# Kernel tuning notes

Measured on AMD Instinct MI355X. Metric: run time of the kernel, lower is better.

Reference implementation:

```python
import jax, jax.numpy as jnp
import numpy as np

B, N, D, H = 2, 2048, 1024, 16
HD = D // H  # 64
EPS = 1e-6


def setup_inputs() -> dict:
    key = jax.random.key(0)
    ks = jax.random.split(key, 16)
    rnd = lambda k, shp: jax.random.normal(k, shp, dtype=jnp.float32)
    w = lambda k, i, o: rnd(k, (i, o)) * 0.02  # stored as (in, out); y = x @ W
    return {
        "x": rnd(ks[0], (B, N, D)),
        "emb_B_D": rnd(ks[1], (B, D)),
        "gate": rnd(ks[2], (B, D)),
        "crossattn_emb": rnd(ks[3], (B, 128, D)),
        "rope_emb_L_1_1_D": rnd(ks[4], (N, HD)),
        "Wq1": w(ks[5], D, D), "Wq2": w(ks[6], D, D),
        "Wk1": w(ks[7], D, D), "Wk2": w(ks[8], D, D),
        "Wv": w(ks[9], D, D),
        "Wo": w(ks[10], D, D),
        "Wada1": w(ks[11], D, D),
        "Wada2": w(ks[12], D, 2 * D),
        "bada2": jnp.zeros((2 * D,), dtype=jnp.float32),
    }


def rotate_half(t):
    t1, t2 = jnp.split(t, 2, axis=-1)
    return jnp.concatenate([-t2, t1], axis=-1)


def reference(x, emb_B_D, gate, crossattn_emb, rope_emb_L_1_1_D,
              Wq1, Wq2, Wk1, Wk2, Wv, Wo, Wada1, Wada2, bada2):
    # adaLN modulation: SiLU -> Linear(no bias) -> Linear(bias)
    ada = jax.nn.silu(emb_B_D) @ Wada1 @ Wada2 + bada2          # [B, 2D]
    shift, scale = jnp.split(ada, 2, axis=1)                    # [B, D] each

    # LayerNorm (no affine) + scale/shift
    mu = jnp.mean(x, axis=-1, keepdims=True)
    var = jnp.var(x, axis=-1, keepdims=True)
    xn = (x - mu) * jax.lax.rsqrt(var + EPS)
    xn = xn * (1.0 + scale[:, None, :]) + shift[:, None, :]     # [B, N, D]

    # QKV projections (each to_q/to_k is two stacked linears, to_v one)
    q = xn @ Wq1 @ Wq2
    k = xn @ Wk1 @ Wk2
    v = xn @ Wv
    split_heads = lambda t: t.reshape(B, N, H, HD).transpose(0, 2, 1, 3)  # b h n d
    q, k, v = split_heads(q), split_heads(k), split_heads(v)

    # RoPE
    cos = jnp.cos(rope_emb_L_1_1_D)[None, None]                 # [1,1,N,HD]
    sin = jnp.sin(rope_emb_L_1_1_D)[None, None]
    q = q * cos + rotate_half(q) * sin
    k = k * cos + rotate_half(k) * sin

    # Attention
    sim = jnp.einsum("bhid,bhjd->bhij", q, k) * (HD ** -0.5)
    attn = jax.nn.softmax(sim, axis=-1)
    out = jnp.einsum("bhij,bhjd->bhid", attn, v)
    out = out.transpose(0, 2, 1, 3).reshape(B, N, D) @ Wo

    # Gated residual
    return x + gate[:, None, :] * out
```

## Files before the change

kernel.cpp:

```cpp
#include <hip/hip_runtime.h>
#include <stdint.h>
#include <math.h>

typedef unsigned short u16;
typedef __attribute__((ext_vector_type(8))) short short8;
typedef __attribute__((ext_vector_type(4))) float f32x4;
typedef __attribute__((ext_vector_type(4))) unsigned short u16x4;
typedef __attribute__((ext_vector_type(2))) unsigned int uint2v;

#define DEV static __device__ __forceinline__

DEV u16 f2bf(float f) {
    unsigned u = __builtin_bit_cast(unsigned, f);
    u = u + 0x7fffu + ((u >> 16) & 1u);
    return (u16)(u >> 16);
}
DEV float bf2f(u16 s) { return __builtin_bit_cast(float, ((unsigned)s) << 16); }
DEV float fexp2(float x) {
#if __has_builtin(__builtin_amdgcn_exp2f)
    return __builtin_amdgcn_exp2f(x);
#else
    return __expf(x * 0.69314718056f);
#endif
}
DEV unsigned cvtpk(float a, float b) {
    unsigned w;
    asm("v_cvt_pk_bf16_f32 %0, %1, %2" : "=v"(w) : "v"(a), "v"(b));
    return w;
}
DEV int xcd_swz(int flat, int nwg) {
    int cpx = nwg >> 3;
    return (flat & 7) * cpx + (flat >> 3);
}

DEV void gl_lds16(const u16* g, u16* l) {
#if __has_builtin(__builtin_amdgcn_global_load_lds)
    __builtin_amdgcn_global_load_lds((const __attribute__((address_space(1))) unsigned int*)g,
                                     (__attribute__((address_space(3))) unsigned int*)l, 16, 0, 0);
#else
    *(short8*)l = *(const short8*)g;
#endif
}


__global__ __launch_bounds__(256) void k_ada1(const float* __restrict__ emb, const float* __restrict__ W,
                                              float* __restrict__ out) {
    int col = blockIdx.x * 64 + (threadIdx.x & 63);
    int b = blockIdx.y;
    int kbase = blockIdx.z * 128 + (threadIdx.x >> 6) * 32;
    float acc = 0.f;
    for (int k = kbase; k < kbase + 32; k++) {
        float e = emb[b * 1024 + k];
        float se = e / (1.f + __expf(-e));
        acc += se * W[(size_t)k * 1024 + col];
    }
    __shared__ float red[4][64];
    red[threadIdx.x >> 6][threadIdx.x & 63] = acc;
    __syncthreads();
    if (threadIdx.x < 64)
        atomicAdd(out + b * 1024 + blockIdx.x * 64 + threadIdx.x,
                  red[0][threadIdx.x] + red[1][threadIdx.x] + red[2][threadIdx.x] + red[3][threadIdx.x]);
}

__global__ __launch_bounds__(256) void k_prep(const float* s0, u16* d0, const float* s1, u16* d1,
                                              const float* s2, u16* d2, const float* s3, u16* d3,
                                              const float* s4, u16* d4, const float* s5, u16* d5,
                                              const float* __restrict__ t_ada, const float* __restrict__ Wada2,
                                              float* __restrict__ ada, const float* __restrict__ rope,
                                              float* __restrict__ cst, float* __restrict__ snt) {
    __shared__ u16 tile[64][65];
    __shared__ float red[4][64];
    if (blockIdx.z == 6) {
        int flat = blockIdx.y * 16 + blockIdx.x;
        int kq = flat >> 6;
        int rest = flat & 63;
        int b = rest >> 5, xb = rest & 31;
        int col = xb * 64 + (threadIdx.x & 63);
        int kbase = kq * 256 + (threadIdx.x >> 6) * 64;
        float acc = 0.f;
        for (int k = kbase; k < kbase + 64; k++)
            acc += t_ada[b * 1024 + k] * Wada2[(size_t)k * 2048 + col];
        red[threadIdx.x >> 6][threadIdx.x & 63] = acc;
        __syncthreads();
        if (threadIdx.x < 64)
            atomicAdd(ada + b * 2048 + xb * 64 + threadIdx.x,
                      red[0][threadIdx.x] + red[1][threadIdx.x] + red[2][threadIdx.x] + red[3][threadIdx.x]);
        return;
    }
    if (blockIdx.z == 7) {
        int flat = blockIdx.y * 16 + blockIdx.x;
        if (flat < 128) {
            int idx = flat * 1024 + threadIdx.x * 4;
            float4 rv = *(const float4*)(rope + idx);
            float4 cv, sv;
            __sincosf(rv.x, &sv.x, &cv.x);
            __sincosf(rv.y, &sv.y, &cv.y);
            __sincosf(rv.z, &sv.z, &cv.z);
            __sincosf(rv.w, &sv.w, &cv.w);
            *(float4*)(cst + idx) = cv;
            *(float4*)(snt + idx) = sv;
        }
        return;
    }
    const float* s; u16* d;
    switch (blockIdx.z) {
        case 0: s = s0; d = d0; break;
        case 1: s = s1; d = d1; break;
        case 2: s = s2; d = d2; break;
        case 3: s = s3; d = d3; break;
        case 4: s = s4; d = d4; break;
        default: s = s5; d = d5; break;
    }
    int k0 = blockIdx.x * 64, n0 = blockIdx.y * 64;
    int tx = threadIdx.x & 63, ty = threadIdx.x >> 6;
    if (blockIdx.z >= 4) {
        #pragma unroll
        for (int i = 0; i < 16; i++) {
            int kk = ty + 4 * i;
            d[(size_t)(k0 + kk) * 1024 + n0 + tx] = f2bf(s[(size_t)(k0 + kk) * 1024 + n0 + tx]);
        }
        return;
    }
    #pragma unroll
    for (int i = 0; i < 16; i++) {
        int kk = ty + 4 * i;
        tile[kk][tx] = f2bf(s[(size_t)(k0 + kk) * 1024 + n0 + tx]);
    }
    __syncthreads();
    #pragma unroll
    for (int i = 0; i < 16; i++) {
        int nn = ty + 4 * i;
        d[(size_t)(n0 + nn) * 1024 + k0 + tx] = tile[tx][nn];
    }
}

__global__ __launch_bounds__(256) void k_ln(const float* __restrict__ x, const float* __restrict__ ada,
                                            const float* __restrict__ bada2, u16* __restrict__ xn) {
    int row = blockIdx.x;
    int b = row >> 11;
    float4 v = ((const float4*)(x + (size_t)row * 1024))[threadIdx.x];
    float s = v.x + v.y + v.z + v.w;
    float ss = v.x * v.x + v.y * v.y + v.z * v.z + v.w * v.w;
    #pragma unroll
    for (int m = 1; m < 64; m <<= 1) { s += __shfl_xor(s, m, 64); ss += __shfl_xor(ss, m, 64); }
    __shared__ float red[2][4];
    int wave = threadIdx.x >> 6, lane = threadIdx.x & 63;
    if (lane == 0) { red[0][wave] = s; red[1][wave] = ss; }
    __syncthreads();
    s = red[0][0] + red[0][1] + red[0][2] + red[0][3];
    ss = red[1][0] + red[1][1] + red[1][2] + red[1][3];
    float mu = s * (1.f / 1024.f);
    float var = ss * (1.f / 1024.f) - mu * mu;
    float rs = rsqrtf(var + 1e-6f);
    int c = threadIdx.x * 4;
    const float* sh = ada + b * 2048;
    const float* sc = ada + b * 2048 + 1024;
    u16x4 r;
    r.x = f2bf((v.x - mu) * rs * (1.f + sc[c + 0] + bada2[1024 + c + 0]) + sh[c + 0] + bada2[c + 0]);
    r.y = f2bf((v.y - mu) * rs * (1.f + sc[c + 1] + bada2[1024 + c + 1]) + sh[c + 1] + bada2[c + 1]);
    r.z = f2bf((v.z - mu) * rs * (1.f + sc[c + 2] + bada2[1024 + c + 2]) + sh[c + 2] + bada2[c + 2]);
    r.w = f2bf((v.w - mu) * rs * (1.f + sc[c + 3] + bada2[1024 + c + 3]) + sh[c + 3] + bada2[c + 3]);
    *(u16x4*)(xn + (size_t)row * 1024 + c) = r;
}

template <int BM, int BN, int MODE>
DEV void gemm_core(const u16* __restrict__ A, const u16* __restrict__ Bt,
                   u16* __restrict__ Cb, float* __restrict__ Cf, u16* __restrict__ Vt,
                   const float* __restrict__ Xres, const float* __restrict__ gate,
                   const float* __restrict__ cst, const float* __restrict__ snt,
                   float scale, int Nn, int K, int m0, int n0) {
    constexpr int MI = BM / 32, NJ = BN / 32;
    constexpr int PA = BM / 64, PB = BN / 64;
    constexpr int LA = BM * 32, LB = BN * 32;
    constexpr int SST = 2 * (LA + LB);
    constexpr int SM = (MODE == 2 && BM * 132 > SST) ? BM * 132 : SST;
    __shared__ u16 smem[SM];
    int tid = threadIdx.x;
    int lane = tid & 63, wave = tid >> 6;
    int wm = (wave & 1) * (BM / 2), wn = (wave >> 1) * (BN / 2);
    int lr = lane & 15, quad = lane >> 4;
    f32x4 acc[MI][NJ];
    #pragma unroll
    for (int i = 0; i < MI; i++)
        #pragma unroll
        for (int j = 0; j < NJ; j++) acc[i][j] = f32x4{0.f, 0.f, 0.f, 0.f};

    int arow = tid >> 2;
    int achunk = (tid & 3) * 8;
    const u16* ap = A + (size_t)(m0 + arow) * K + achunk;
    const u16* bp = Bt + (size_t)(n0 + arow) * K + achunk;

    auto stage = [&](int it, int d) {
        int koff = it * 32;
        int ab = d * LA, bb = 2 * LA + d * LB;
        #pragma unroll
        for (int p = 0; p < PA; p++)
            gl_lds16(ap + koff + (size_t)(64 * p) * K, smem + ab + (arow + 64 * p) * 32 + achunk);
        #pragma unroll
        for (int p = 0; p < PB; p++)
            gl_lds16(bp + koff + (size_t)(64 * p) * K, smem + bb + (arow + 64 * p) * 32 + achunk);
    };

    stage(0, 0);
    __syncthreads();
    #pragma unroll 1
    for (int it = 0; it < 32; ++it) {
        int cur = it & 1;
        if (it + 1 < 32) stage(it + 1, cur ^ 1);
        int ab = cur * LA, bb = 2 * LA + cur * LB;
        short8 af[MI], bfr[NJ];
        #pragma unroll
        for (int i = 0; i < MI; i++)
            af[i] = *(const short8*)(smem + ab + (wm + i * 16 + lr) * 32 + quad * 8);
        #pragma unroll
        for (int j = 0; j < NJ; j++)
            bfr[j] = *(const short8*)(smem + bb + (wn + j * 16 + lr) * 32 + quad * 8);
        #pragma unroll
        for (int i = 0; i < MI; i++)
            #pragma unroll
            for (int j = 0; j < NJ; j++)
                acc[i][j] = __builtin_amdgcn_mfma_f32_16x16x32_bf16(af[i], bfr[j], acc[i][j], 0, 0, 0);
        __syncthreads();
    }

    if (MODE == 2) {
        if ((n0 + wn) < 2048) {
            #pragma unroll
            for (int i = 0; i < MI; i++)
                #pragma unroll
                for (int jp = 0; jp < 2; jp++)
                    #pragma unroll
                    for (int r = 0; r < 4; r++) {
                        int row = m0 + wm + i * 16 + quad * 4 + r;
                        int n = row & 2047;
                        int d1 = jp * 16 + lr;
                        float c1 = cst[n * 64 + d1],      s1 = snt[n * 64 + d1];
                        float c2 = cst[n * 64 + d1 + 32], s2 = snt[n * 64 + d1 + 32];
                        float x1 = acc[i][jp][r], x2 = acc[i][jp + 2][r];
                        Cb[(size_t)row * Nn + n0 + wn + d1]      = f2bf(x1 * c1 - x2 * s1);
                        Cb[(size_t)row * Nn + n0 + wn + d1 + 32] = f2bf(x2 * c2 + x1 * s2);
                    }
        } else {
            #pragma unroll
            for (int i = 0; i < MI; i++)
                #pragma unroll
                for (int j = 0; j < NJ; j++) {
                    u16x4 w;
                    w.x = f2bf(acc[i][j][0]); w.y = f2bf(acc[i][j][1]);
                    w.z = f2bf(acc[i][j][2]); w.w = f2bf(acc[i][j][3]);
                    *(u16x4*)(&smem[(wn + j * 16 + lr) * 132 + wm + i * 16 + quad * 4]) = w;
                }
            __syncthreads();
            int d = tid >> 1, half = tid & 1;
            int gcol = n0 - 2048 + d;
            int hv = gcol >> 6, dl = gcol & 63;
            int bb2 = m0 >> 11;
            int nloc = (m0 & 2047) + half * 64;
            u16* dst = Vt + ((size_t)((bb2 * 16 + hv) * 64 + dl)) * 2048 + nloc;
            #pragma unroll
            for (int c = 0; c < 8; c++)
                *(short8*)(dst + c * 8) = *(const short8*)(&smem[d * 132 + half * 64 + c * 8]);
        }
        return;
    }
    #pragma unroll
    for (int i = 0; i < MI; i++)
        #pragma unroll
        for (int j = 0; j < NJ; j++)
            #pragma unroll
            for (int r = 0; r < 4; r++) {
                int row = m0 + wm + i * 16 + quad * 4 + r;
                int col = n0 + wn + j * 16 + lr;
                float v = acc[i][j][r];
                if (MODE == 1) {
                    int b = row >> 11;
                    Cf[(size_t)row * Nn + col] = Xres[(size_t)row * Nn + col] + gate[b * 1024 + col] * v;
                } else {
                    Cb[(size_t)row * Nn + col] = f2bf(v * scale);
                }
            }
}

template <int BM, int BN, int MODE, int WPE>
__global__ __launch_bounds__(256, WPE) void gemm_bt(const u16* __restrict__ A, const u16* __restrict__ Bt,
                                                    u16* __restrict__ Cb, float* __restrict__ Cf,
                                                    u16* __restrict__ Vt,
                                                    const float* __restrict__ Xres, const float* __restrict__ gate,
                                                    const float* __restrict__ cst, const float* __restrict__ snt,
                                                    int Nn, int K) {
    int gx = gridDim.x;
    int flat = blockIdx.y * gx + blockIdx.x;
    int swz = xcd_swz(flat, gx * gridDim.y);
    gemm_core<BM, BN, MODE>(A, Bt, Cb, Cf, Vt, Xres, gate, cst, snt, 1.f, Nn, K,
                            (swz / gx) * BM, (swz % gx) * BN);
}

__global__ __launch_bounds__(256, 4) void gemm_fold(const u16* A0, const u16* B0, u16* C0,
                                                    const u16* A1, const u16* B1, u16* C1) {
    const u16* A = blockIdx.z ? A1 : A0;
    const u16* Bt = blockIdx.z ? B1 : B0;
    u16* C = blockIdx.z ? C1 : C0;
    float scale = blockIdx.z ? 1.0f : 0.18033688f;
    int flat = blockIdx.y * 16 + blockIdx.x;
    int swz = xcd_swz(flat, 128);
    gemm_core<128, 64, 0>(A, Bt, C, nullptr, nullptr, nullptr, nullptr, nullptr, nullptr, scale,
                          1024, 1024, (swz >> 4) * 128, (swz & 15) * 64);
}

__global__ __launch_bounds__(512) void k_attn(const u16* __restrict__ qkv, const u16* __restrict__ vt,
                                              u16* __restrict__ aob) {
    __shared__ u16 pool[128 * 72];
    __shared__ u16 Ks[2][64][64];
    __shared__ u16 Vs[2][64][64];
    int flat = blockIdx.y * 16 + blockIdx.x;
    int swz = xcd_swz(flat, 512);
    int q0 = (swz & 15) * 128;
    int bh = swz >> 4; int b = bh >> 4, h = bh & 15;
    int tid = threadIdx.x;
    int lane = tid & 63, wave = tid >> 6;
    int lr = lane & 15, quad = lane >> 4;
    int srow = tid >> 3, scol = (tid & 7) * 8;
    int sg = (((tid & 7) ^ (srow & 7))) * 8;
    int cc[2] = { ((quad ^ (lr & 7))) * 8, (((4 + quad) ^ (lr & 7))) * 8 };
    int qrow = wave * 16 + lr;

    const u16* kp = qkv + ((size_t)(b * 2048 + srow)) * 2048 + 1024 + h * 64 + sg;
    const u16* vp = vt + ((size_t)(bh * 64 + srow)) * 2048 + sg;

    #pragma unroll
    for (int p = 0; p < 2; p++)
        gl_lds16(qkv + ((size_t)(b * 2048 + q0 + srow + 64 * p)) * 2048 + h * 64 + sg,
                 pool + (srow + 64 * p) * 64 + scol);

    short8 krA, vrA, krB, vrB;
    krA = *(const short8*)(kp);
    vrA = *(const short8*)(vp);
    __syncthreads();
    short8 qf[2];
    #pragma unroll
    for (int ks = 0; ks < 2; ks++)
        qf[ks] = *(const short8*)(pool + qrow * 64 + cc[ks]);
    *(short8*)(&Ks[0][srow][scol]) = krA;
    *(short8*)(&Vs[0][srow][scol]) = vrA;
    krB = *(const short8*)(kp + (size_t)64 * 2048);
    vrB = *(const short8*)(vp + 64);
    __syncthreads();

    float l_part = 0.f;
    f32x4 oacc[4];
    #pragma unroll
    for (int dt = 0; dt < 4; dt++) oacc[dt] = f32x4{0.f, 0.f, 0.f, 0.f};

    auto body = [&](int it, int cur, short8& krF, short8& vrF, short8& krH, short8& vrH) {
        if (it < 30) {
            krF = *(const short8*)(kp + (size_t)(it + 2) * 64 * 2048);
            vrF = *(const short8*)(vp + (it + 2) * 64);
        }
        f32x4 st[4];
        #pragma unroll
        for (int ct = 0; ct < 4; ct++) st[ct] = f32x4{0.f, 0.f, 0.f, 0.f};
        #pragma unroll
        for (int ks = 0; ks < 2; ks++) {
            short8 kf[4];
            #pragma unroll
            for (int ct = 0; ct < 4; ct++)
                kf[ct] = *(const short8*)(&Ks[cur][ct * 16 + lr][cc[ks]]);
            __builtin_amdgcn_s_setprio(1);
            #pragma unroll
            for (int ct = 0; ct < 4; ct++)
                st[ct] = __builtin_amdgcn_mfma_f32_16x16x32_bf16(kf[ct], qf[ks], st[ct], 0, 0, 0);
            __builtin_amdgcn_s_setprio(0);
        }
        #pragma unroll
        for (int ct = 0; ct < 4; ct++) {
            float p0 = fexp2(st[ct][0]);
            float p1 = fexp2(st[ct][1]);
            float p2 = fexp2(st[ct][2]);
            float p3 = fexp2(st[ct][3]);
            l_part += (p0 + p1) + (p2 + p3);
            uint2v w; w.x = cvtpk(p0, p1); w.y = cvtpk(p2, p3);
            *(uint2v*)(pool + qrow * 72 + ct * 16 + quad * 4) = w;
        }
        #pragma unroll
        for (int ks = 0; ks < 2; ks++) {
            short8 pf, vf[4];
            pf = *(const short8*)(pool + qrow * 72 + ks * 32 + quad * 8);
            #pragma unroll
            for (int dt = 0; dt < 4; dt++)
                vf[dt] = *(const short8*)(&Vs[cur][dt * 16 + lr][cc[ks]]);
            __builtin_amdgcn_s_setprio(1);
            #pragma unroll
            for (int dt = 0; dt < 4; dt++)
                oacc[dt] = __builtin_amdgcn_mfma_f32_16x16x32_bf16(pf, vf[dt], oacc[dt], 0, 0, 0);
            __builtin_amdgcn_s_setprio(0);
        }
        if (it < 31) {
            int nxt = cur ^ 1;
            *(short8*)(&Ks[nxt][srow][scol]) = krH;
            *(short8*)(&Vs[nxt][srow][scol]) = vrH;
        }
        __syncthreads();
    };

    #pragma unroll 1
    for (int it2 = 0; it2 < 16; ++it2) {
        body(2 * it2,     0, krA, vrA, krB, vrB);
        body(2 * it2 + 1, 1, krB, vrB, krA, vrA);
    }

    float l = l_part;
    l += __shfl_xor(l, 16, 64);
    l += __shfl_xor(l, 32, 64);
    float linv[4];
    #pragma unroll
    for (int r = 0; r < 4; r++)
        linv[r] = 1.f / __shfl(l, quad * 4 + r, 64);
    #pragma unroll
    for (int dt = 0; dt < 4; dt++)
        #pragma unroll
        for (int r = 0; r < 4; r++) {
            int row = q0 + wave * 16 + quad * 4 + r;
            aob[((size_t)(b * 2048 + row)) * 1024 + h * 64 + dt * 16 + lr] =
                f2bf(oacc[dt][r] * linv[r]);
        }
}

extern "C" void kernel_launch(void* const* d_in, const int* in_sizes, int n_in,
                              void* d_out, int out_size, void* d_ws, size_t ws_size,
                              hipStream_t stream) {
    const float* x     = (const float*)d_in[0];
    const float* emb   = (const float*)d_in[1];
    const float* gate  = (const float*)d_in[2];
    const float* rope  = (const float*)d_in[4];
    const float* Wq1   = (const float*)d_in[5];
    const float* Wq2   = (const float*)d_in[6];
    const float* Wk1   = (const float*)d_in[7];
    const float* Wk2   = (const float*)d_in[8];
    const float* Wv    = (const float*)d_in[9];
    const float* Wo    = (const float*)d_in[10];
    const float* Wada1 = (const float*)d_in[11];
    const float* Wada2 = (const float*)d_in[12];
    const float* bada2 = (const float*)d_in[13];
    float* out = (float*)d_out;

    char* ws = (char*)d_ws;
    size_t off = 0;
    auto alloc = [&](size_t bytes) { void* p = ws + off; off += (bytes + 255) & ~(size_t)255; return p; };
    float* t_ada = (float*)alloc(2048 * 4);
    float* ada   = (float*)alloc(4096 * 4);
    float* cst   = (float*)alloc((size_t)131072 * 4);
    float* snt   = (float*)alloc((size_t)131072 * 4);
    u16* xn    = (u16*)alloc((size_t)4096 * 1024 * 2);
    u16* Wq1b  = (u16*)alloc((size_t)1024 * 1024 * 2);
    u16* Wk1b  = (u16*)alloc((size_t)1024 * 1024 * 2);
    u16* Wq2t  = (u16*)alloc((size_t)1024 * 1024 * 2);
    u16* Wk2t  = (u16*)alloc((size_t)1024 * 1024 * 2);
    u16* Wot   = (u16*)alloc((size_t)1024 * 1024 * 2);
    u16* WqkvT = (u16*)alloc((size_t)3072 * 1024 * 2);
    u16* qkvb  = (u16*)alloc((size_t)4096 * 2048 * 2);
    u16* vtb   = (u16*)alloc((size_t)4096 * 1024 * 2);
    u16* aob   = (u16*)alloc((size_t)4096 * 1024 * 2);
    (void)ws_size; (void)in_sizes; (void)n_in; (void)out_size;

    hipMemsetAsync(t_ada, 0, 2048 * 4, stream);
    hipMemsetAsync(ada, 0, 4096 * 4, stream);

    k_ada1<<<dim3(16, 2, 8), 256, 0, stream>>>(emb, Wada1, t_ada);

    k_prep<<<dim3(16, 16, 8), 256, 0, stream>>>(Wq2, Wq2t, Wk2, Wk2t,
                                                Wv, WqkvT + (size_t)2048 * 1024, Wo, Wot,
                                                Wq1, Wq1b, Wk1, Wk1b,
                                                t_ada, Wada2, ada, rope, cst, snt);

    k_ln<<<4096, 256, 0, stream>>>(x, ada, bada2, xn);

    gemm_fold<<<dim3(16, 8, 2), 256, 0, stream>>>(Wq2t, Wq1b, WqkvT,
                                                  Wk2t, Wk1b, WqkvT + (size_t)1024 * 1024);

    gemm_bt<128, 128, 2, 4><<<dim3(24, 32), 256, 0, stream>>>(xn, WqkvT, qkvb, nullptr, vtb,
                                                              nullptr, nullptr, cst, snt, 2048, 1024);

    k_attn<<<dim3(16, 32), 512, 0, stream>>>(qkvb, vtb, aob);

    gemm_bt<128, 64, 1, 4><<<dim3(16, 32), 256, 0, stream>>>(aob, Wot, nullptr, out, nullptr, x, gate,
                                                             nullptr, nullptr, 1024, 1024);
}
```

Baseline: 256.5 us.

## Triple-buffer GEMM LDS stages with vmcnt-based waits and lighter barriers

The GEMM main loop moves from a double-buffered to a triple-buffered LDS pipeline. It issues global-to-LDS loads two k-steps ahead and waits with a partial vmcnt count, so one stage's loads can still be in flight at each barrier. The attention loop's __syncthreads is replaced by an explicit lgkmcnt(0) wait plus s_barrier, which avoids draining outstanding vector-memory loads. The cost is 1.5x more shared memory per GEMM block, which may lower occupancy, and the hand-written waitcnt logic must stay correct.

Measured after the change: 257.2 us. About the same (+0.3%).

```diff
diff --git a/kernel.cpp b/kernel.cpp
--- a/kernel.cpp
+++ b/kernel.cpp
@@ -40,6 +40,12 @@
 #else
     *(short8*)l = *(const short8*)g;
 #endif
+}
+
+DEV void barrier_lgkm() {
+    asm volatile("s_waitcnt lgkmcnt(0)" ::: "memory");
+    __builtin_amdgcn_sched_barrier(0);
+    __builtin_amdgcn_s_barrier();
 }
 
 
@@ -172,7 +178,8 @@
     constexpr int MI = BM / 32, NJ = BN / 32;
     constexpr int PA = BM / 64, PB = BN / 64;
     constexpr int LA = BM * 32, LB = BN * 32;
-    constexpr int SST = 2 * (LA + LB);
+    constexpr int LBUF = LA + LB;
+    constexpr int SST = 3 * LBUF;
     constexpr int SM = (MODE == 2 && BM * 132 > SST) ? BM * 132 : SST;
     __shared__ u16 smem[SM];
     int tid = threadIdx.x;
@@ -192,7 +199,7 @@
 
     auto stage = [&](int it, int d) {
         int koff = it * 32;
-        int ab = d * LA, bb = 2 * LA + d * LB;
+        int ab = d * LBUF, bb = d * LBUF + LA;
         #pragma unroll
         for (int p = 0; p < PA; p++)
             gl_lds16(ap + koff + (size_t)(64 * p) * K, smem + ab + (arow + 64 * p) * 32 + achunk);
@@ -202,12 +209,15 @@
     };
 
     stage(0, 0);
-    __syncthreads();
+    stage(1, 1);
+    asm volatile("s_waitcnt vmcnt(%0)" :: "i"(PA + PB) : "memory");
+    __builtin_amdgcn_sched_barrier(0);
+    __builtin_amdgcn_s_barrier();
     #pragma unroll 1
     for (int it = 0; it < 32; ++it) {
-        int cur = it & 1;
-        if (it + 1 < 32) stage(it + 1, cur ^ 1);
-        int ab = cur * LA, bb = 2 * LA + cur * LB;
+        int cur = it % 3;
+        if (it + 2 < 32) stage(it + 2, (it + 2) % 3);
+        int ab = cur * LBUF, bb = ab + LA;
         short8 af[MI], bfr[NJ];
         #pragma unroll
         for (int i = 0; i < MI; i++)
@@ -220,8 +230,16 @@
             #pragma unroll
             for (int j = 0; j < NJ; j++)
                 acc[i][j] = __builtin_amdgcn_mfma_f32_16x16x32_bf16(af[i], bfr[j], acc[i][j], 0, 0, 0);
-        __syncthreads();
-    }
+        if (it + 1 < 32) {
+            if (it + 2 < 32)
+                asm volatile("s_waitcnt vmcnt(%0)" :: "i"(PA + PB) : "memory");
+            else
+                asm volatile("s_waitcnt vmcnt(0)" ::: "memory");
+            __builtin_amdgcn_sched_barrier(0);
+            __builtin_amdgcn_s_barrier();
+        }
+    }
+    __syncthreads();
 
     if (MODE == 2) {
         if ((n0 + wn) < 2048) {
@@ -399,7 +417,7 @@
             *(short8*)(&Ks[nxt][srow][scol]) = krH;
             *(short8*)(&Vs[nxt][srow][scol]) = vrH;
         }
-        __syncthreads();
+        barrier_lgkm();
     };
 
     #pragma unroll 1
```

## Use 512-thread GEMM blocks with 4x2 wave grid and lighter attention barrier

Applied to the files above, without the earlier changes.

The GEMM kernels move from 256 to 512 threads, laid out as a 4x2 wave grid. Each wave now computes half as many M tiles, so it needs fewer accumulators and gets more latency hiding. Tile staging is rewritten so each thread issues one load per operand, and the shared-memory layout and V-transpose write-out are adjusted to match. The attention loop's __syncthreads is replaced by an explicit lgkmcnt wait plus a raw s_barrier, and two memsets are merged into one. The trade-off is more waves per block that must synchronise, and fewer MFMAs per wave for each LDS load.

Measured after the change: 255.9 us. About the same (-0.3%).

```diff
diff --git a/kernel.cpp b/kernel.cpp
--- a/kernel.cpp
+++ b/kernel.cpp
@@ -40,6 +40,12 @@
 #else
     *(short8*)l = *(const short8*)g;
 #endif
+}
+
+DEV void barrier_lgkm() {
+    asm volatile("s_waitcnt lgkmcnt(0)" ::: "memory");
+    __builtin_amdgcn_sched_barrier(0);
+    __builtin_amdgcn_s_barrier();
 }
 
 
@@ -169,15 +175,15 @@
                    const float* __restrict__ Xres, const float* __restrict__ gate,
                    const float* __restrict__ cst, const float* __restrict__ snt,
                    float scale, int Nn, int K, int m0, int n0) {
-    constexpr int MI = BM / 32, NJ = BN / 32;
-    constexpr int PA = BM / 64, PB = BN / 64;
+    constexpr int MI = BM / 64, NJ = BN / 32;
     constexpr int LA = BM * 32, LB = BN * 32;
-    constexpr int SST = 2 * (LA + LB);
+    constexpr int LBUF = LA + LB;
+    constexpr int SST = 2 * LBUF;
     constexpr int SM = (MODE == 2 && BM * 132 > SST) ? BM * 132 : SST;
     __shared__ u16 smem[SM];
     int tid = threadIdx.x;
     int lane = tid & 63, wave = tid >> 6;
-    int wm = (wave & 1) * (BM / 2), wn = (wave >> 1) * (BN / 2);
+    int wm = (wave & 3) * (BM / 4), wn = (wave >> 2) * (BN / 2);
     int lr = lane & 15, quad = lane >> 4;
     f32x4 acc[MI][NJ];
     #pragma unroll
@@ -192,13 +198,11 @@
 
     auto stage = [&](int it, int d) {
         int koff = it * 32;
-        int ab = d * LA, bb = 2 * LA + d * LB;
-        #pragma unroll
-        for (int p = 0; p < PA; p++)
-            gl_lds16(ap + koff + (size_t)(64 * p) * K, smem + ab + (arow + 64 * p) * 32 + achunk);
-        #pragma unroll
-        for (int p = 0; p < PB; p++)
-            gl_lds16(bp + koff + (size_t)(64 * p) * K, smem + bb + (arow + 64 * p) * 32 + achunk);
+        int ab = d * LBUF, bb = d * LBUF + LA;
+        if (tid < BM * 4)
+            gl_lds16(ap + koff, smem + ab + arow * 32 + achunk);
+        if (tid < BN * 4)
+            gl_lds16(bp + koff, smem + bb + arow * 32 + achunk);
     };
 
     stage(0, 0);
@@ -207,7 +211,7 @@
     for (int it = 0; it < 32; ++it) {
         int cur = it & 1;
         if (it + 1 < 32) stage(it + 1, cur ^ 1);
-        int ab = cur * LA, bb = 2 * LA + cur * LB;
+        int ab = cur * LBUF, bb = ab + LA;
         short8 af[MI], bfr[NJ];
         #pragma unroll
         for (int i = 0; i < MI; i++)
@@ -251,15 +255,15 @@
                     *(u16x4*)(&smem[(wn + j * 16 + lr) * 132 + wm + i * 16 + quad * 4]) = w;
                 }
             __syncthreads();
-            int d = tid >> 1, half = tid & 1;
+            int d = tid >> 2, q4 = tid & 3;
             int gcol = n0 - 2048 + d;
             int hv = gcol >> 6, dl = gcol & 63;
             int bb2 = m0 >> 11;
-            int nloc = (m0 & 2047) + half * 64;
+            int nloc = (m0 & 2047) + q4 * 32;
             u16* dst = Vt + ((size_t)((bb2 * 16 + hv) * 64 + dl)) * 2048 + nloc;
             #pragma unroll
-            for (int c = 0; c < 8; c++)
-                *(short8*)(dst + c * 8) = *(const short8*)(&smem[d * 132 + half * 64 + c * 8]);
+            for (int c = 0; c < 4; c++)
+                *(short8*)(dst + c * 8) = *(const short8*)(&smem[d * 132 + q4 * 32 + c * 8]);
         }
         return;
     }
@@ -282,7 +286,7 @@
 }
 
 template <int BM, int BN, int MODE, int WPE>
-__global__ __launch_bounds__(256, WPE) void gemm_bt(const u16* __restrict__ A, const u16* __restrict__ Bt,
+__global__ __launch_bounds__(512, WPE) void gemm_bt(const u16* __restrict__ A, const u16* __restrict__ Bt,
                                                     u16* __restrict__ Cb, float* __restrict__ Cf,
                                                     u16* __restrict__ Vt,
                                                     const float* __restrict__ Xres, const float* __restrict__ gate,
@@ -295,7 +299,7 @@
                             (swz / gx) * BM, (swz % gx) * BN);
 }
 
-__global__ __launch_bounds__(256, 4) void gemm_fold(const u16* A0, const u16* B0, u16* C0,
+__global__ __launch_bounds__(512, 4) void gemm_fold(const u16* A0, const u16* B0, u16* C0,
                                                     const u16* A1, const u16* B1, u16* C1) {
     const u16* A = blockIdx.z ? A1 : A0;
     const u16* Bt = blockIdx.z ? B1 : B0;
@@ -399,7 +403,7 @@
             *(short8*)(&Ks[nxt][srow][scol]) = krH;
             *(short8*)(&Vs[nxt][srow][scol]) = vrH;
         }
-        __syncthreads();
+        barrier_lgkm();
     };
 
     #pragma unroll 1
@@ -462,8 +466,7 @@
     u16* aob   = (u16*)alloc((size_t)4096 * 1024 * 2);
     (void)ws_size; (void)in_sizes; (void)n_in; (void)out_size;
 
-    hipMemsetAsync(t_ada, 0, 2048 * 4, stream);
-    hipMemsetAsync(ada, 0, 4096 * 4, stream);
+    hipMemsetAsync(t_ada, 0, 24576, stream);
 
     k_ada1<<<dim3(16, 2, 8), 256, 0, stream>>>(emb, Wada1, t_ada);
 
@@ -474,14 +477,14 @@
 
     k_ln<<<4096, 256, 0, stream>>>(x, ada, bada2, xn);
 
-    gemm_fold<<<dim3(16, 8, 2), 256, 0, stream>>>(Wq2t, Wq1b, WqkvT,
+    gemm_fold<<<dim3(16, 8, 2), 512, 0, stream>>>(Wq2t, Wq1b, WqkvT,
                                                   Wk2t, Wk1b, WqkvT + (size_t)1024 * 1024);
 
-    gemm_bt<128, 128, 2, 4><<<dim3(24, 32), 256, 0, stream>>>(xn, WqkvT, qkvb, nullptr, vtb,
+    gemm_bt<128, 128, 2, 4><<<dim3(24, 32), 512, 0, stream>>>(xn, WqkvT, qkvb, nullptr, vtb,
                                                               nullptr, nullptr, cst, snt, 2048, 1024);
 
     k_attn<<<dim3(16, 32), 512, 0, stream>>>(qkvb, vtb, aob);
 
-    gemm_bt<128, 64, 1, 4><<<dim3(16, 32), 256, 0, stream>>>(aob, Wot, nullptr, out, nullptr, x, gate,
+    gemm_bt<128, 64, 1, 4><<<dim3(16, 32), 512, 0, stream>>>(aob, Wot, nullptr, out, nullptr, x, gate,
                                                              nullptr, nullptr, 1024, 1024);
 }
```
